# Kernel optimization log

Hardware: AMD Instinct MI355X
Metric: run time of the kernel (lower is better)

## Reference

```python
import jax, jax.numpy as jnp
import numpy as np

SIGMA = 2.0      # test_cfg.sigma (gaussian kernel)
MASK_THR = 0.5   # test_cfg.mask_thr
NUM_CLASSES = 80


def setup_inputs() -> dict:
    key = jax.random.key(0)
    k1, k2, k3 = jax.random.split(key, 3)
    N, H, W = 500, 200, 304  # nms_pre instances, mask-feat resolution (stride-4 of 800x1216)
    mask_preds = jax.random.uniform(k1, (N, H, W), dtype=jnp.float32)
    labels = jax.random.randint(k2, (N,), 0, NUM_CLASSES, dtype=jnp.int32)
    scores = jax.random.uniform(k3, (N,), dtype=jnp.float32)
    return {"mask_preds": mask_preds, "labels": labels, "scores": scores}


def reference(mask_preds, labels, scores):
    """Matrix NMS (gaussian kernel) as in mask_matrix_nms with filter_thr=-1, max_num=-1.

    mask_preds: (N, H, W) sigmoid probabilities; thresholded at MASK_THR to binary masks
    labels:     (N,) int32 class ids
    scores:     (N,) float32 classification scores
    Returns (scores, labels, masks, keep_inds) with fixed shape N.
    """
    N = scores.shape[0]
    masks = (mask_preds > MASK_THR).astype(jnp.float32)           # (N,H,W) binary
    mask_area = masks.sum((1, 2))                                  # (N,)

    # sort by score, descending
    order = jnp.argsort(-scores)
    scores_s = scores[order]
    masks_s = masks[order]
    area_s = mask_area[order]
    labels_s = labels[order]

    flat = masks_s.reshape(N, -1)                                  # (N, H*W)
    inter = flat @ flat.T                                          # (N,N) intersection
    union = area_s[:, None] + area_s[None, :] - inter
    iou = jnp.triu(inter / union, k=1)                             # (N,N) upper-tri IoU

    label_eq = jnp.triu((labels_s[:, None] == labels_s[None, :]).astype(jnp.float32), k=1)
    decay_iou = iou * label_eq                                     # same-class IoU

    compensate_iou = decay_iou.max(axis=0)                         # (N,) max IoU w/ higher-scored same-class mask
    decay_matrix = jnp.exp(-SIGMA * decay_iou ** 2)                # (N,N)
    compensate_matrix = jnp.exp(-SIGMA * compensate_iou ** 2)[:, None]  # broadcast along rows (torch transpose)
    decay_coefficient = (decay_matrix / compensate_matrix).min(axis=0)  # (N,)

    scores_decayed = scores_s * decay_coefficient

    # final sort by decayed score, descending
    order2 = jnp.argsort(-scores_decayed)
    out_scores = scores_decayed[order2]
    out_labels = labels_s[order2]
    out_masks = masks_s[order2]
    keep_inds = order[order2]
    return out_scores, out_labels, out_masks, keep_inds
```

## Files before the change

### kernel.cpp

```cpp
#include <hip/hip_runtime.h>

typedef unsigned long long ull;

constexpr int N   = 500;
constexpr int HW  = 60800;
constexpr int NW  = 950;
constexpr int NC  = 80;
constexpr int NTILES = N * NW / 4;
constexpr int PB  = 1024;
constexpr int QPB = (HW / 4 + 255) / 256;

__global__ void __launch_bounds__(512)
k_packsort(const float* __restrict__ mp, const int* __restrict__ labels,
           const float* __restrict__ scores,
           ull* __restrict__ packed, int* __restrict__ order_g,
           float* __restrict__ scoresS_g, int* __restrict__ labelsS_g,
           int* __restrict__ offs_g, int* __restrict__ members_g,
           int2* __restrict__ pairList, int* __restrict__ pairCount_g) {
    const int t    = threadIdx.x;
    const int lane = t & 63;

    if (blockIdx.x != 0) {
        int wid    = (blockIdx.x - 1) * 8 + (t >> 6);
        int nwaves = PB * 8;
        for (int tile = wid; tile < NTILES; tile += nwaves) {
            size_t base = (size_t)tile * 256;
            float v0 = mp[base +   0 + lane];
            float v1 = mp[base +  64 + lane];
            float v2 = mp[base + 128 + lane];
            float v3 = mp[base + 192 + lane];
            ull b0 = __ballot(v0 > 0.5f);
            ull b1 = __ballot(v1 > 0.5f);
            ull b2 = __ballot(v2 > 0.5f);
            ull b3 = __ballot(v3 > 0.5f);
            if (lane == 0) {
                longlong4 w;
                w.x = (long long)b0; w.y = (long long)b1;
                w.z = (long long)b2; w.w = (long long)b3;
                *(longlong4*)(packed + tile * 4) = w;
            }
        }
        return;
    }

    __shared__ float sS[N];
    __shared__ int   orderS[N];
    __shared__ int   labS[N];
    __shared__ int   cnt[NC];
    __shared__ int   offs[NC + 1];
    __shared__ int   members[N];
    __shared__ int   pcnt;

    if (t < N) sS[t] = scores[t];
    if (t < NC) cnt[t] = 0;
    if (t == 0) pcnt = 0;
    __syncthreads();
    if (t < N) {
        float si = sS[t];
        int rank = 0;
        for (int j = 0; j < N; ++j) {
            float sj = sS[j];
            if (sj > si || (sj == si && j < t)) rank++;
        }
        orderS[rank] = t;
    }
    __syncthreads();
    if (t < N) {
        int o = orderS[t];
        order_g[t]   = o;
        scoresS_g[t] = sS[o];
        int l = labels[o];
        labS[t] = l;
        labelsS_g[t] = l;
    }
    __syncthreads();
    if (t < N) atomicAdd(&cnt[labS[t]], 1);
    __syncthreads();
    if (t == 0) {
        int s = 0;
        for (int c = 0; c < NC; ++c) { offs[c] = s; s += cnt[c]; }
        offs[NC] = s;
    }
    __syncthreads();
    if (t < NC) cnt[t] = offs[t];
    __syncthreads();
    if (t < N) { int p = atomicAdd(&cnt[labS[t]], 1); members[p] = t; }
    __syncthreads();
    if (t < NC) {
        int b = offs[t], e = offs[t + 1];
        for (int a = b; a < e; ++a)
            for (int c2 = a + 1; c2 < e; ++c2) {
                int i = members[a], j = members[c2];
                int lo = min(i, j), hi = max(i, j);
                int p = atomicAdd(&pcnt, 1);
                pairList[p] = make_int2(lo, hi);
            }
    }
    __syncthreads();
    if (t <= NC) offs_g[t] = offs[t];
    if (t < N)   members_g[t] = members[t];
    if (t == 0)  *pairCount_g = pcnt;
}

__global__ void k_iou(const ull* __restrict__ packed, const int* __restrict__ order,
                      const int* __restrict__ pairCount, const int2* __restrict__ pairList,
                      float* __restrict__ iou) {
    int gw     = (blockIdx.x * blockDim.x + threadIdx.x) >> 6;
    int lane   = threadIdx.x & 63;
    int nwaves = (gridDim.x * blockDim.x) >> 6;
    int np     = *pairCount;
    for (int p = gw; p < np; p += nwaves) {
        int2 pr = pairList[p];
        const ull* A = packed + (size_t)order[pr.x] * NW;
        const ull* B = packed + (size_t)order[pr.y] * NW;
        ull acc = 0;
        for (int w = lane; w < NW; w += 64) {
            ull a = A[w], b = B[w];
            acc += (ull)__popcll(a & b)
                 + ((ull)__popcll(a) << 21)
                 + ((ull)__popcll(b) << 42);
        }
#pragma unroll
        for (int off = 32; off > 0; off >>= 1) acc += __shfl_down(acc, off, 64);
        if (lane == 0) {
            float inter = (float)(int)(acc & 0x1FFFFF);
            float areaA = (float)(int)((acc >> 21) & 0x1FFFFF);
            float areaB = (float)(int)((acc >> 42) & 0x1FFFFF);
            float uni   = areaA + areaB - inter;
            iou[pr.x * N + pr.y] = inter / uni;
        }
    }
}

__global__ void __launch_bounds__(512)
k_decay(const int* __restrict__ labelsS_g, const float* __restrict__ scoresS_g,
        const int* __restrict__ offs_g, const int* __restrict__ members_g,
        const int* __restrict__ order_g, const float* __restrict__ iou,
        float* __restrict__ outScores, float* __restrict__ outLabels,
        float* __restrict__ outKeep, int* __restrict__ keepOrig_g) {
    __shared__ int   labS[N];
    __shared__ float compS[N];
    __shared__ float sdec[N];
    __shared__ int   offs[NC + 1];
    __shared__ int   members[N];
    int t = threadIdx.x;
    if (t < N)  { labS[t] = labelsS_g[t]; members[t] = members_g[t]; }
    if (t <= NC) offs[t] = offs_g[t];
    __syncthreads();
    if (t < N) {
        int lj = labS[t];
        float m = 0.f;
        int b = offs[lj], e = offs[lj + 1];
        for (int q = b; q < e; ++q) {
            int i = members[q];
            if (i < t) m = fmaxf(m, iou[i * N + t]);
        }
        compS[t] = m;
    }
    __syncthreads();
    if (t < N) {
        int lj = labS[t];
        float c = 1.f;
        int b = offs[lj], e = offs[lj + 1];
        for (int q = b; q < e; ++q) {
            int i = members[q];
            if (i < t) {
                float d  = iou[i * N + t];
                float ci = compS[i];
                c = fminf(c, expf(-2.f * d * d) / expf(-2.f * ci * ci));
            }
        }
        sdec[t] = scoresS_g[t] * c;
    }
    __syncthreads();
    if (t < N) {
        float sj = sdec[t];
        int rank = 0;
        for (int i = 0; i < N; ++i) {
            float si = sdec[i];
            if (si > sj || (si == sj && i < t)) rank++;
        }
        int o = order_g[t];
        outScores[rank]  = sj;
        outLabels[rank]  = (float)labS[t];
        outKeep[rank]    = (float)o;
        keepOrig_g[rank] = o;
    }
}

__global__ void k_gather(const ull* __restrict__ packed, const int* __restrict__ keepOrig,
                         float4* __restrict__ outMasks) {
    int q = blockIdx.x * blockDim.x + threadIdx.x;
    if (q >= HW / 4) return;
    int k    = blockIdx.y;
    int orig = keepOrig[k];
    int pix  = q * 4;
    ull w  = packed[(size_t)orig * NW + (pix >> 6)];
    int sh = pix & 63;
    float4 r;
    r.x = (float)((w >> (sh    )) & 1ULL);
    r.y = (float)((w >> (sh + 1)) & 1ULL);
    r.z = (float)((w >> (sh + 2)) & 1ULL);
    r.w = (float)((w >> (sh + 3)) & 1ULL);
    outMasks[(size_t)k * (HW / 4) + q] = r;
}

extern "C" void kernel_launch(void* const* d_in, const int* in_sizes, int n_in,
                              void* d_out, int out_size, void* d_ws, size_t ws_size,
                              hipStream_t stream) {
    const float* mask_preds = (const float*)d_in[0];
    const int*   labels     = (const int*)d_in[1];
    const float* scores     = (const float*)d_in[2];

    float*  o         = (float*)d_out;
    float*  outScores = o;
    float*  outLabels = o + N;
    float4* outMasks  = (float4*)(o + 2 * N);
    float*  outKeep   = o + 2 * N + (size_t)N * HW;

    char* w = (char*)d_ws;
    ull*   packed     = (ull*)w;   w += (size_t)N * NW * 8;
    int*   order_g    = (int*)w;   w += N * 4;
    float* scoresS_g  = (float*)w; w += N * 4;
    int*   labelsS_g  = (int*)w;   w += N * 4;
    int*   offs_g     = (int*)w;   w += (NC + 4) * 4;
    int*   members_g  = (int*)w;   w += N * 4;
    int*   keepOrig_g = (int*)w;   w += N * 4;
    int*   pairCount  = (int*)w;   w += 16;
    int2*  pairList   = (int2*)w;  w += (size_t)(N * (N - 1) / 2) * 8;
    float* iou        = (float*)w;

    hipLaunchKernelGGL(k_packsort, dim3(PB + 1), dim3(512), 0, stream,
                       mask_preds, labels, scores, packed, order_g,
                       scoresS_g, labelsS_g, offs_g, members_g, pairList, pairCount);
    hipLaunchKernelGGL(k_iou, dim3(256), dim3(256), 0, stream,
                       packed, order_g, pairCount, pairList, iou);
    hipLaunchKernelGGL(k_decay, dim3(1), dim3(512), 0, stream,
                       labelsS_g, scoresS_g, offs_g, members_g, order_g, iou,
                       outScores, outLabels, outKeep, keepOrig_g);
    hipLaunchKernelGGL(k_gather, dim3(QPB, N), dim3(256), 0, stream,
                       packed, keepOrig_g, outMasks);
}
```

Baseline: 88.57 us.

## Fuse pack/sort, IoU, and decay kernels into one launch with atomic grid sync

```diff
diff --git a/kernel.cpp b/kernel.cpp
--- a/kernel.cpp
+++ b/kernel.cpp
@@ -8,22 +8,36 @@
 constexpr int NC  = 80;
 constexpr int NTILES = N * NW / 4;
 constexpr int PB  = 1024;
+constexpr int G   = PB + 1;
+constexpr int TAIL = 64;
 constexpr int QPB = (HW / 4 + 255) / 256;
 
 __global__ void __launch_bounds__(512)
-k_packsort(const float* __restrict__ mp, const int* __restrict__ labels,
-           const float* __restrict__ scores,
-           ull* __restrict__ packed, int* __restrict__ order_g,
-           float* __restrict__ scoresS_g, int* __restrict__ labelsS_g,
-           int* __restrict__ offs_g, int* __restrict__ members_g,
-           int2* __restrict__ pairList, int* __restrict__ pairCount_g) {
+k_fused(const float* __restrict__ mp, const int* __restrict__ labels,
+        const float* __restrict__ scores,
+        ull* __restrict__ packed, int* __restrict__ order_g,
+        float* __restrict__ scoresS_g, int* __restrict__ labelsS_g,
+        int* __restrict__ offs_g, int* __restrict__ members_g,
+        int2* __restrict__ pairList, int* __restrict__ pairCount_g,
+        float* __restrict__ iou, int* __restrict__ done1, int* __restrict__ done2,
+        float* __restrict__ outScores, float* __restrict__ outLabels,
+        float* __restrict__ outKeep, int* __restrict__ keepOrig_g) {
     const int t    = threadIdx.x;
     const int lane = t & 63;
 
+    __shared__ float fbufA[N];
+    __shared__ float fbufB[N];
+    __shared__ int   ibufA[N];
+    __shared__ int   ibufB[N];
+    __shared__ int   ibufC[NC + 1];
+    __shared__ int   cntS[NC];
+    __shared__ int   pcnt;
+    __shared__ int   role;
+    __shared__ int   isLast;
+
     if (blockIdx.x != 0) {
-        int wid    = (blockIdx.x - 1) * 8 + (t >> 6);
-        int nwaves = PB * 8;
-        for (int tile = wid; tile < NTILES; tile += nwaves) {
+        int wid = (blockIdx.x - 1) * 8 + (t >> 6);
+        for (int tile = wid; tile < NTILES; tile += PB * 8) {
             size_t base = (size_t)tile * 256;
             float v0 = mp[base +   0 + lane];
             float v1 = mp[base +  64 + lane];
@@ -40,151 +54,166 @@
                 *(longlong4*)(packed + tile * 4) = w;
             }
         }
-        return;
-    }
-
-    __shared__ float sS[N];
-    __shared__ int   orderS[N];
-    __shared__ int   labS[N];
-    __shared__ int   cnt[NC];
-    __shared__ int   offs[NC + 1];
-    __shared__ int   members[N];
-    __shared__ int   pcnt;
-
-    if (t < N) sS[t] = scores[t];
-    if (t < NC) cnt[t] = 0;
-    if (t == 0) pcnt = 0;
-    __syncthreads();
-    if (t < N) {
-        float si = sS[t];
-        int rank = 0;
-        for (int j = 0; j < N; ++j) {
-            float sj = sS[j];
-            if (sj > si || (sj == si && j < t)) rank++;
-        }
-        orderS[rank] = t;
-    }
-    __syncthreads();
-    if (t < N) {
-        int o = orderS[t];
-        order_g[t]   = o;
-        scoresS_g[t] = sS[o];
-        int l = labels[o];
-        labS[t] = l;
-        labelsS_g[t] = l;
-    }
-    __syncthreads();
-    if (t < N) atomicAdd(&cnt[labS[t]], 1);
+    } else {
+        float* sS     = fbufA;
+        int*   orderS = ibufA;
+        int*   labS   = ibufB;
+        int*   offs   = ibufC;
+        if (t < N) sS[t] = scores[t];
+        if (t < NC) cntS[t] = 0;
+        if (t == 0) pcnt = 0;
+        __syncthreads();
+        if (t < N) {
+            float si = sS[t];
+            int rank = 0;
+            for (int j = 0; j < N; ++j) {
+                float sj = sS[j];
+                if (sj > si || (sj == si && j < t)) rank++;
+            }
+            orderS[rank] = t;
+        }
+        __syncthreads();
+        int myLab = -1;
+        if (t < N) {
+            int o = orderS[t];
+            order_g[t]   = o;
+            scoresS_g[t] = sS[o];
+            myLab = labels[o];
+            labS[t] = myLab;
+            labelsS_g[t] = myLab;
+        }
+        __syncthreads();
+        if (t < N) atomicAdd(&cntS[myLab], 1);
+        __syncthreads();
+        if (t == 0) {
+            int s = 0;
+            for (int c = 0; c < NC; ++c) { offs[c] = s; s += cntS[c]; }
+            offs[NC] = s;
+        }
+        __syncthreads();
+        if (t < NC) cntS[t] = offs[t];
+        __syncthreads();
+        int* members = ibufA;
+        if (t < N) { int p = atomicAdd(&cntS[myLab], 1); members[p] = t; }
+        __syncthreads();
+        if (t < NC) {
+            int b = offs[t], e = offs[t + 1];
+            for (int a = b; a < e; ++a)
+                for (int c2 = a + 1; c2 < e; ++c2) {
+                    int i = members[a], j = members[c2];
+                    int lo = min(i, j), hi = max(i, j);
+                    int p = atomicAdd(&pcnt, 1);
+                    pairList[p] = make_int2(lo, hi);
+                }
+        }
+        __syncthreads();
+        if (t <= NC) offs_g[t] = offs[t];
+        if (t < N)   members_g[t] = members[t];
+        if (t == 0)  *pairCount_g = pcnt;
+    }
+
+    __threadfence();
     __syncthreads();
     if (t == 0) {
-        int s = 0;
-        for (int c = 0; c < NC; ++c) { offs[c] = s; s += cnt[c]; }
-        offs[NC] = s;
-    }
-    __syncthreads();
-    if (t < NC) cnt[t] = offs[t];
-    __syncthreads();
-    if (t < N) { int p = atomicAdd(&cnt[labS[t]], 1); members[p] = t; }
-    __syncthreads();
-    if (t < NC) {
-        int b = offs[t], e = offs[t + 1];
-        for (int a = b; a < e; ++a)
-            for (int c2 = a + 1; c2 < e; ++c2) {
-                int i = members[a], j = members[c2];
-                int lo = min(i, j), hi = max(i, j);
-                int p = atomicAdd(&pcnt, 1);
-                pairList[p] = make_int2(lo, hi);
-            }
-    }
-    __syncthreads();
-    if (t <= NC) offs_g[t] = offs[t];
-    if (t < N)   members_g[t] = members[t];
-    if (t == 0)  *pairCount_g = pcnt;
-}
-
-__global__ void k_iou(const ull* __restrict__ packed, const int* __restrict__ order,
-                      const int* __restrict__ pairCount, const int2* __restrict__ pairList,
-                      float* __restrict__ iou) {
-    int gw     = (blockIdx.x * blockDim.x + threadIdx.x) >> 6;
-    int lane   = threadIdx.x & 63;
-    int nwaves = (gridDim.x * blockDim.x) >> 6;
-    int np     = *pairCount;
-    for (int p = gw; p < np; p += nwaves) {
-        int2 pr = pairList[p];
-        const ull* A = packed + (size_t)order[pr.x] * NW;
-        const ull* B = packed + (size_t)order[pr.y] * NW;
-        ull acc = 0;
-        for (int w = lane; w < NW; w += 64) {
-            ull a = A[w], b = B[w];
-            acc += (ull)__popcll(a & b)
-                 + ((ull)__popcll(a) << 21)
-                 + ((ull)__popcll(b) << 42);
-        }
+        int old = __hip_atomic_fetch_add(done1, 1, __ATOMIC_ACQ_REL,
+                                         __HIP_MEMORY_SCOPE_AGENT);
+        int r = old - (G - TAIL);
+        if (r >= 0) {
+            while (__hip_atomic_load(done1, __ATOMIC_RELAXED,
+                                     __HIP_MEMORY_SCOPE_AGENT) < G)
+                __builtin_amdgcn_s_sleep(2);
+        }
+        role = r;
+    }
+    __syncthreads();
+    if (role < 0) return;
+    __threadfence();
+
+    {
+        int gw = role * 8 + (t >> 6);
+        int np = *pairCount_g;
+        for (int p = gw; p < np; p += TAIL * 8) {
+            int2 pr = pairList[p];
+            const ull* A = packed + (size_t)order_g[pr.x] * NW;
+            const ull* B = packed + (size_t)order_g[pr.y] * NW;
+            ull acc = 0;
+            for (int w = lane; w < NW; w += 64) {
+                ull a = A[w], b = B[w];
+                acc += (ull)__popcll(a & b)
+                     + ((ull)__popcll(a) << 21)
+                     + ((ull)__popcll(b) << 42);
+            }
 #pragma unroll
-        for (int off = 32; off > 0; off >>= 1) acc += __shfl_down(acc, off, 64);
-        if (lane == 0) {
-            float inter = (float)(int)(acc & 0x1FFFFF);
-            float areaA = (float)(int)((acc >> 21) & 0x1FFFFF);
-            float areaB = (float)(int)((acc >> 42) & 0x1FFFFF);
-            float uni   = areaA + areaB - inter;
-            iou[pr.x * N + pr.y] = inter / uni;
-        }
-    }
-}
-
-__global__ void __launch_bounds__(512)
-k_decay(const int* __restrict__ labelsS_g, const float* __restrict__ scoresS_g,
-        const int* __restrict__ offs_g, const int* __restrict__ members_g,
-        const int* __restrict__ order_g, const float* __restrict__ iou,
-        float* __restrict__ outScores, float* __restrict__ outLabels,
-        float* __restrict__ outKeep, int* __restrict__ keepOrig_g) {
-    __shared__ int   labS[N];
-    __shared__ float compS[N];
-    __shared__ float sdec[N];
-    __shared__ int   offs[NC + 1];
-    __shared__ int   members[N];
-    int t = threadIdx.x;
-    if (t < N)  { labS[t] = labelsS_g[t]; members[t] = members_g[t]; }
-    if (t <= NC) offs[t] = offs_g[t];
-    __syncthreads();
-    if (t < N) {
-        int lj = labS[t];
-        float m = 0.f;
-        int b = offs[lj], e = offs[lj + 1];
-        for (int q = b; q < e; ++q) {
-            int i = members[q];
-            if (i < t) m = fmaxf(m, iou[i * N + t]);
-        }
-        compS[t] = m;
-    }
-    __syncthreads();
-    if (t < N) {
-        int lj = labS[t];
-        float c = 1.f;
-        int b = offs[lj], e = offs[lj + 1];
-        for (int q = b; q < e; ++q) {
-            int i = members[q];
-            if (i < t) {
-                float d  = iou[i * N + t];
-                float ci = compS[i];
-                c = fminf(c, expf(-2.f * d * d) / expf(-2.f * ci * ci));
-            }
-        }
-        sdec[t] = scoresS_g[t] * c;
-    }
-    __syncthreads();
-    if (t < N) {
-        float sj = sdec[t];
-        int rank = 0;
-        for (int i = 0; i < N; ++i) {
-            float si = sdec[i];
-            if (si > sj || (si == sj && i < t)) rank++;
-        }
-        int o = order_g[t];
-        outScores[rank]  = sj;
-        outLabels[rank]  = (float)labS[t];
-        outKeep[rank]    = (float)o;
-        keepOrig_g[rank] = o;
+            for (int off = 32; off > 0; off >>= 1) acc += __shfl_down(acc, off, 64);
+            if (lane == 0) {
+                float inter = (float)(int)(acc & 0x1FFFFF);
+                float areaA = (float)(int)((acc >> 21) & 0x1FFFFF);
+                float areaB = (float)(int)((acc >> 42) & 0x1FFFFF);
+                float uni   = areaA + areaB - inter;
+                iou[pr.x * N + pr.y] = inter / uni;
+            }
+        }
+    }
+
+    __threadfence();
+    __syncthreads();
+    if (t == 0) {
+        int old2 = __hip_atomic_fetch_add(done2, 1, __ATOMIC_ACQ_REL,
+                                          __HIP_MEMORY_SCOPE_AGENT);
+        isLast = (old2 == TAIL - 1);
+    }
+    __syncthreads();
+    if (!isLast) return;
+    __threadfence();
+
+    {
+        int*   labS    = ibufB;
+        int*   members = ibufA;
+        int*   offs    = ibufC;
+        float* compS   = fbufA;
+        float* sdec    = fbufB;
+        if (t < N)  { labS[t] = labelsS_g[t]; members[t] = members_g[t]; }
+        if (t <= NC) offs[t] = offs_g[t];
+        __syncthreads();
+        if (t < N) {
+            int lj = labS[t];
+            float m = 0.f;
+            int b = offs[lj], e = offs[lj + 1];
+            for (int q = b; q < e; ++q) {
+                int i = members[q];
+                if (i < t) m = fmaxf(m, iou[i * N + t]);
+            }
+            compS[t] = m;
+        }
+        __syncthreads();
+        if (t < N) {
+            int lj = labS[t];
+            float c = 1.f;
+            int b = offs[lj], e = offs[lj + 1];
+            for (int q = b; q < e; ++q) {
+                int i = members[q];
+                if (i < t) {
+                    float d  = iou[i * N + t];
+                    float ci = compS[i];
+                    c = fminf(c, expf(-2.f * d * d) / expf(-2.f * ci * ci));
+                }
+            }
+            sdec[t] = scoresS_g[t] * c;
+        }
+        __syncthreads();
+        if (t < N) {
+            float sj = sdec[t];
+            int rank = 0;
+            for (int i = 0; i < N; ++i) {
+                float si = sdec[i];
+                if (si > sj || (si == sj && i < t)) rank++;
+            }
+            int o = order_g[t];
+            outScores[rank]  = sj;
+            outLabels[rank]  = (float)labS[t];
+            outKeep[rank]    = (float)o;
+            keepOrig_g[rank] = o;
+        }
     }
 }
 
@@ -226,17 +255,20 @@
     int*   offs_g     = (int*)w;   w += (NC + 4) * 4;
     int*   members_g  = (int*)w;   w += N * 4;
     int*   keepOrig_g = (int*)w;   w += N * 4;
-    int*   pairCount  = (int*)w;   w += 16;
-    int2*  pairList   = (int2*)w;  w += (size_t)(N * (N - 1) / 2) * 8;
-    float* iou        = (float*)w;
-
-    hipLaunchKernelGGL(k_packsort, dim3(PB + 1), dim3(512), 0, stream,
+    int*   counters   = (int*)w;   w += 128;
+    float* iou        = (float*)w; w += (size_t)N * N * 4;
+    int2*  pairList   = (int2*)w;
+
+    int* done1     = counters;
+    int* done2     = counters + 1;
+    int* pairCount = counters + 2;
+
+    hipMemsetAsync(counters, 0, 128, stream);
+
+    hipLaunchKernelGGL(k_fused, dim3(G), dim3(512), 0, stream,
                        mask_preds, labels, scores, packed, order_g,
-                       scoresS_g, labelsS_g, offs_g, members_g, pairList, pairCount);
-    hipLaunchKernelGGL(k_iou, dim3(256), dim3(256), 0, stream,
-                       packed, order_g, pairCount, pairList, iou);
-    hipLaunchKernelGGL(k_decay, dim3(1), dim3(512), 0, stream,
-                       labelsS_g, scoresS_g, offs_g, members_g, order_g, iou,
+                       scoresS_g, labelsS_g, offs_g, members_g, pairList, pairCount,
+                       iou, done1, done2,
                        outScores, outLabels, outKeep, keepOrig_g);
     hipLaunchKernelGGL(k_gather, dim3(QPB, N), dim3(256), 0, stream,
                        packed, keepOrig_g, outMasks);
```

New measurement: 324.3 us. 266% more time.

## Fuse IoU, decay and mask gather into one persistent ticketed kernel

Applied to the files above, without the earlier changes.

```diff
diff --git a/kernel.cpp b/kernel.cpp
--- a/kernel.cpp
+++ b/kernel.cpp
@@ -8,7 +8,8 @@
 constexpr int NC  = 80;
 constexpr int NTILES = N * NW / 4;
 constexpr int PB  = 1024;
-constexpr int QPB = (HW / 4 + 255) / 256;
+constexpr int NB2 = 576;
+constexpr int IOUB = 64;
 
 __global__ void __launch_bounds__(512)
 k_packsort(const float* __restrict__ mp, const int* __restrict__ labels,
@@ -16,14 +17,14 @@
            ull* __restrict__ packed, int* __restrict__ order_g,
            float* __restrict__ scoresS_g, int* __restrict__ labelsS_g,
            int* __restrict__ offs_g, int* __restrict__ members_g,
-           int2* __restrict__ pairList, int* __restrict__ pairCount_g) {
+           int2* __restrict__ pairList, int* __restrict__ counters,
+           int* __restrict__ keepOrig_g) {
     const int t    = threadIdx.x;
     const int lane = t & 63;
 
     if (blockIdx.x != 0) {
-        int wid    = (blockIdx.x - 1) * 8 + (t >> 6);
-        int nwaves = PB * 8;
-        for (int tile = wid; tile < NTILES; tile += nwaves) {
+        int wid = (blockIdx.x - 1) * 8 + (t >> 6);
+        for (int tile = wid; tile < NTILES; tile += PB * 8) {
             size_t base = (size_t)tile * 256;
             float v0 = mp[base +   0 + lane];
             float v1 = mp[base +  64 + lane];
@@ -51,6 +52,8 @@
     __shared__ int   members[N];
     __shared__ int   pcnt;
 
+    if (t < N) keepOrig_g[t] = -1;
+    if (t < 3) counters[t] = 0;
     if (t < N) sS[t] = scores[t];
     if (t < NC) cnt[t] = 0;
     if (t == 0) pcnt = 0;
@@ -65,16 +68,17 @@
         orderS[rank] = t;
     }
     __syncthreads();
+    int myLab = -1;
     if (t < N) {
         int o = orderS[t];
         order_g[t]   = o;
         scoresS_g[t] = sS[o];
-        int l = labels[o];
-        labS[t] = l;
-        labelsS_g[t] = l;
-    }
-    __syncthreads();
-    if (t < N) atomicAdd(&cnt[labS[t]], 1);
+        myLab = labels[o];
+        labS[t] = myLab;
+        labelsS_g[t] = myLab;
+    }
+    __syncthreads();
+    if (t < N) atomicAdd(&cnt[myLab], 1);
     __syncthreads();
     if (t == 0) {
         int s = 0;
@@ -84,7 +88,7 @@
     __syncthreads();
     if (t < NC) cnt[t] = offs[t];
     __syncthreads();
-    if (t < N) { int p = atomicAdd(&cnt[labS[t]], 1); members[p] = t; }
+    if (t < N) { int p = atomicAdd(&cnt[myLab], 1); members[p] = t; }
     __syncthreads();
     if (t < NC) {
         int b = offs[t], e = offs[t + 1];
@@ -99,110 +103,150 @@
     __syncthreads();
     if (t <= NC) offs_g[t] = offs[t];
     if (t < N)   members_g[t] = members[t];
-    if (t == 0)  *pairCount_g = pcnt;
+    if (t == 0)  counters[3] = pcnt;
 }
 
-__global__ void k_iou(const ull* __restrict__ packed, const int* __restrict__ order,
-                      const int* __restrict__ pairCount, const int2* __restrict__ pairList,
-                      float* __restrict__ iou) {
-    int gw     = (blockIdx.x * blockDim.x + threadIdx.x) >> 6;
-    int lane   = threadIdx.x & 63;
-    int nwaves = (gridDim.x * blockDim.x) >> 6;
-    int np     = *pairCount;
-    for (int p = gw; p < np; p += nwaves) {
-        int2 pr = pairList[p];
-        const ull* A = packed + (size_t)order[pr.x] * NW;
-        const ull* B = packed + (size_t)order[pr.y] * NW;
-        ull acc = 0;
-        for (int w = lane; w < NW; w += 64) {
-            ull a = A[w], b = B[w];
-            acc += (ull)__popcll(a & b)
-                 + ((ull)__popcll(a) << 21)
-                 + ((ull)__popcll(b) << 42);
-        }
+__global__ void __launch_bounds__(512)
+k_iougather(const ull* __restrict__ packed, const int* __restrict__ order_g,
+            const float* __restrict__ scoresS_g, const int* __restrict__ labelsS_g,
+            const int* __restrict__ offs_g, const int* __restrict__ members_g,
+            const int2* __restrict__ pairList, int* __restrict__ counters,
+            int* __restrict__ iouI, int* __restrict__ keepOrig_g,
+            float* __restrict__ outScores, float* __restrict__ outLabels,
+            float* __restrict__ outKeep, float4* __restrict__ outMasks) {
+    const int t    = threadIdx.x;
+    const int lane = t & 63;
+    int* ticket1 = counters + 0;
+    int* ticket2 = counters + 1;
+    int* wq      = counters + 2;
+
+    __shared__ int sRole, sLast, sUnit, sOrig;
+
+    if (t == 0) sRole = __hip_atomic_fetch_add(ticket1, 1, __ATOMIC_RELAXED,
+                                               __HIP_MEMORY_SCOPE_AGENT);
+    __syncthreads();
+
+    if (sRole < IOUB) {
+        int np = counters[3];
+        for (int p = sRole * 8 + (t >> 6); p < np; p += IOUB * 8) {
+            int2 pr = pairList[p];
+            const ull* A = packed + (size_t)order_g[pr.x] * NW;
+            const ull* B = packed + (size_t)order_g[pr.y] * NW;
+            ull acc = 0;
+            for (int w = lane; w < NW; w += 64) {
+                ull a = A[w], b = B[w];
+                acc += (ull)__popcll(a & b)
+                     + ((ull)__popcll(a) << 21)
+                     + ((ull)__popcll(b) << 42);
+            }
 #pragma unroll
-        for (int off = 32; off > 0; off >>= 1) acc += __shfl_down(acc, off, 64);
-        if (lane == 0) {
-            float inter = (float)(int)(acc & 0x1FFFFF);
-            float areaA = (float)(int)((acc >> 21) & 0x1FFFFF);
-            float areaB = (float)(int)((acc >> 42) & 0x1FFFFF);
-            float uni   = areaA + areaB - inter;
-            iou[pr.x * N + pr.y] = inter / uni;
-        }
-    }
-}
-
-__global__ void __launch_bounds__(512)
-k_decay(const int* __restrict__ labelsS_g, const float* __restrict__ scoresS_g,
-        const int* __restrict__ offs_g, const int* __restrict__ members_g,
-        const int* __restrict__ order_g, const float* __restrict__ iou,
-        float* __restrict__ outScores, float* __restrict__ outLabels,
-        float* __restrict__ outKeep, int* __restrict__ keepOrig_g) {
-    __shared__ int   labS[N];
-    __shared__ float compS[N];
-    __shared__ float sdec[N];
-    __shared__ int   offs[NC + 1];
-    __shared__ int   members[N];
-    int t = threadIdx.x;
-    if (t < N)  { labS[t] = labelsS_g[t]; members[t] = members_g[t]; }
-    if (t <= NC) offs[t] = offs_g[t];
-    __syncthreads();
-    if (t < N) {
-        int lj = labS[t];
-        float m = 0.f;
-        int b = offs[lj], e = offs[lj + 1];
-        for (int q = b; q < e; ++q) {
-            int i = members[q];
-            if (i < t) m = fmaxf(m, iou[i * N + t]);
-        }
-        compS[t] = m;
-    }
-    __syncthreads();
-    if (t < N) {
-        int lj = labS[t];
-        float c = 1.f;
-        int b = offs[lj], e = offs[lj + 1];
-        for (int q = b; q < e; ++q) {
-            int i = members[q];
-            if (i < t) {
-                float d  = iou[i * N + t];
-                float ci = compS[i];
-                c = fminf(c, expf(-2.f * d * d) / expf(-2.f * ci * ci));
-            }
-        }
-        sdec[t] = scoresS_g[t] * c;
-    }
-    __syncthreads();
-    if (t < N) {
-        float sj = sdec[t];
-        int rank = 0;
-        for (int i = 0; i < N; ++i) {
-            float si = sdec[i];
-            if (si > sj || (si == sj && i < t)) rank++;
-        }
-        int o = order_g[t];
-        outScores[rank]  = sj;
-        outLabels[rank]  = (float)labS[t];
-        outKeep[rank]    = (float)o;
-        keepOrig_g[rank] = o;
-    }
-}
-
-__global__ void k_gather(const ull* __restrict__ packed, const int* __restrict__ keepOrig,
-                         float4* __restrict__ outMasks) {
-    int q = blockIdx.x * blockDim.x + threadIdx.x;
-    if (q >= HW / 4) return;
-    int k    = blockIdx.y;
-    int orig = keepOrig[k];
-    int pix  = q * 4;
-    ull w  = packed[(size_t)orig * NW + (pix >> 6)];
-    int sh = pix & 63;
-    float4 r;
-    r.x = (float)((w >> (sh    )) & 1ULL);
-    r.y = (float)((w >> (sh + 1)) & 1ULL);
-    r.z = (float)((w >> (sh + 2)) & 1ULL);
-    r.w = (float)((w >> (sh + 3)) & 1ULL);
-    outMasks[(size_t)k * (HW / 4) + q] = r;
+            for (int off = 32; off > 0; off >>= 1) acc += __shfl_down(acc, off, 64);
+            if (lane == 0) {
+                float inter = (float)(int)(acc & 0x1FFFFF);
+                float areaA = (float)(int)((acc >> 21) & 0x1FFFFF);
+                float areaB = (float)(int)((acc >> 42) & 0x1FFFFF);
+                float uni   = areaA + areaB - inter;
+                __hip_atomic_store(iouI + pr.x * N + pr.y,
+                                   __float_as_int(inter / uni),
+                                   __ATOMIC_RELAXED, __HIP_MEMORY_SCOPE_AGENT);
+            }
+        }
+        asm volatile("s_waitcnt vmcnt(0)" ::: "memory");
+        __syncthreads();
+        if (t == 0) sLast = __hip_atomic_fetch_add(ticket2, 1, __ATOMIC_RELAXED,
+                                                   __HIP_MEMORY_SCOPE_AGENT);
+        __syncthreads();
+
+        if (sLast == IOUB - 1) {
+            __shared__ int   labS[N];
+            __shared__ float compS[N];
+            __shared__ float sdec[N];
+            __shared__ int   offs[NC + 1];
+            __shared__ int   members[N];
+            if (t < N)  { labS[t] = labelsS_g[t]; members[t] = members_g[t]; }
+            if (t <= NC) offs[t] = offs_g[t];
+            __syncthreads();
+            if (t < N) {
+                int lj = labS[t];
+                float m = 0.f;
+                int b = offs[lj], e = offs[lj + 1];
+                for (int q = b; q < e; ++q) {
+                    int i = members[q];
+                    if (i < t) {
+                        float v = __int_as_float(__hip_atomic_load(
+                            iouI + i * N + t, __ATOMIC_RELAXED,
+                            __HIP_MEMORY_SCOPE_AGENT));
+                        m = fmaxf(m, v);
+                    }
+                }
+                compS[t] = m;
+            }
+            __syncthreads();
+            if (t < N) {
+                int lj = labS[t];
+                float c = 1.f;
+                int b = offs[lj], e = offs[lj + 1];
+                for (int q = b; q < e; ++q) {
+                    int i = members[q];
+                    if (i < t) {
+                        float d = __int_as_float(__hip_atomic_load(
+                            iouI + i * N + t, __ATOMIC_RELAXED,
+                            __HIP_MEMORY_SCOPE_AGENT));
+                        float ci = compS[i];
+                        c = fminf(c, expf(-2.f * d * d) / expf(-2.f * ci * ci));
+                    }
+                }
+                sdec[t] = scoresS_g[t] * c;
+            }
+            __syncthreads();
+            if (t < N) {
+                float sj = sdec[t];
+                int rank = 0;
+                for (int i = 0; i < N; ++i) {
+                    float si = sdec[i];
+                    if (si > sj || (si == sj && i < t)) rank++;
+                }
+                int o = order_g[t];
+                outScores[rank] = sj;
+                outLabels[rank] = (float)labS[t];
+                outKeep[rank]   = (float)o;
+                __hip_atomic_store(keepOrig_g + rank, o, __ATOMIC_RELAXED,
+                                   __HIP_MEMORY_SCOPE_AGENT);
+            }
+            __syncthreads();
+        }
+    }
+
+    for (;;) {
+        if (t == 0) sUnit = __hip_atomic_fetch_add(wq, 1, __ATOMIC_RELAXED,
+                                                   __HIP_MEMORY_SCOPE_AGENT);
+        __syncthreads();
+        int k = sUnit;
+        if (k >= N) break;
+        if (t == 0) {
+            int v;
+            while ((v = __hip_atomic_load(keepOrig_g + k, __ATOMIC_RELAXED,
+                                          __HIP_MEMORY_SCOPE_AGENT)) < 0)
+                __builtin_amdgcn_s_sleep(16);
+            sOrig = v;
+        }
+        __syncthreads();
+        int orig = sOrig;
+        const ull* row = packed + (size_t)orig * NW;
+        float4*    dst = outMasks + (size_t)k * (HW / 4);
+        for (int q = t; q < HW / 4; q += 512) {
+            int pix = q * 4;
+            ull w  = row[pix >> 6];
+            int sh = pix & 63;
+            float4 r;
+            r.x = (float)((w >> (sh    )) & 1ULL);
+            r.y = (float)((w >> (sh + 1)) & 1ULL);
+            r.z = (float)((w >> (sh + 2)) & 1ULL);
+            r.w = (float)((w >> (sh + 3)) & 1ULL);
+            dst[q] = r;
+        }
+        __syncthreads();
+    }
 }
 
 extern "C" void kernel_launch(void* const* d_in, const int* in_sizes, int n_in,
@@ -226,18 +270,16 @@
     int*   offs_g     = (int*)w;   w += (NC + 4) * 4;
     int*   members_g  = (int*)w;   w += N * 4;
     int*   keepOrig_g = (int*)w;   w += N * 4;
-    int*   pairCount  = (int*)w;   w += 16;
-    int2*  pairList   = (int2*)w;  w += (size_t)(N * (N - 1) / 2) * 8;
-    float* iou        = (float*)w;
+    int*   counters   = (int*)w;   w += 128;
+    int*   iouI       = (int*)w;   w += (size_t)N * N * 4;
+    int2*  pairList   = (int2*)w;
 
     hipLaunchKernelGGL(k_packsort, dim3(PB + 1), dim3(512), 0, stream,
                        mask_preds, labels, scores, packed, order_g,
-                       scoresS_g, labelsS_g, offs_g, members_g, pairList, pairCount);
-    hipLaunchKernelGGL(k_iou, dim3(256), dim3(256), 0, stream,
-                       packed, order_g, pairCount, pairList, iou);
-    hipLaunchKernelGGL(k_decay, dim3(1), dim3(512), 0, stream,
-                       labelsS_g, scoresS_g, offs_g, members_g, order_g, iou,
-                       outScores, outLabels, outKeep, keepOrig_g);
-    hipLaunchKernelGGL(k_gather, dim3(QPB, N), dim3(256), 0, stream,
-                       packed, keepOrig_g, outMasks);
+                       scoresS_g, labelsS_g, offs_g, members_g, pairList,
+                       counters, keepOrig_g);
+    hipLaunchKernelGGL(k_iougather, dim3(NB2), dim3(512), 0, stream,
+                       packed, order_g, scoresS_g, labelsS_g, offs_g, members_g,
+                       pairList, counters, iouI, keepOrig_g,
+                       outScores, outLabels, outKeep, outMasks);
 }
```

New measurement: 110.6 us. +24.9%, slower.
